# Kernel optimization log

Measured on AMD Instinct MI355X. Metric: run time of the kernel, lower is better.

Reference implementation:

```python
import jax, jax.numpy as jnp
import numpy as np
from jax import lax

N = 4096
T = 8192
DT = 0.1
C_M = 1.0
E_REST = 0.0
G_M_LEAK = 5.0
I_BIAS = 0.0


def setup_inputs() -> dict:
    key = jax.random.key(0)
    i_ext_vector = jax.random.normal(key, (N, T), dtype=jnp.float32)
    return {"i_ext_vector": i_ext_vector}


def reference(i_ext_vector) -> jnp.ndarray:
    # RK2 (modified Euler) integration of leaky non-spiking neuron dynamics.
    # dv/dt = (i_bias + i_ext - (v - e_rest) * g_m_leak) / c_m
    def dvdt(v, i_ext):
        return (I_BIAS + i_ext - (v - E_REST) * G_M_LEAK) / C_M

    def step(v, i_t):
        k1 = dvdt(v, i_t)
        k2 = dvdt(v + 0.5 * DT * k1, i_t)
        v_new = v + DT * k2
        return v_new, v_new

    v0 = jnp.full((N,), E_REST, dtype=i_ext_vector.dtype)
    # scan over time: i_ext_vector is (N, T) -> scan over leading axis of (T, N)
    _, v_hist = lax.scan(step, v0, i_ext_vector.T)  # v_hist: (T, N)
    return v_hist.T  # (N, T), matches v_m_Post
```

## Files before the change

kernel.cpp:

```cpp
#include <hip/hip_runtime.h>


typedef float fx4 __attribute__((ext_vector_type(4)));

constexpr int TT  = 8192;
constexpr int BLK = 256;
constexpr int SEG = 2048;
constexpr int NV  = 8;
constexpr int WPB = BLK / 64;

__global__ __launch_bounds__(BLK, 4)
void neuron_scan(const float* __restrict__ in, float* __restrict__ out,
                 int nseg) {
    const float A    = 0.625f;
    const float Bc   = 0.075f;
    const float A4   = 0.152587890625f;
    const float A8   = 2.32830643653869629e-2f;
    const float A16  = 5.42101086242752217e-4f;
    const float A32  = 2.93873587705571877e-7f;
    const float A64  = 8.63616855509444463e-14f;
    const float A128 = 7.45834073120020674e-27f;

    const int lane = threadIdx.x & 63;
    const int wid  = blockIdx.x * WPB + (threadIdx.x >> 6);
    const int nw   = gridDim.x * WPB;

    for (int s = wid; s < nseg; s += nw) {
        const int row = s >> 2;
        const int col = s & 3;
        const size_t base = (size_t)row * TT + (size_t)col * SEG;
        const fx4* src = (const fx4*)(in + base);

        fx4 x[NV];
        #pragma unroll
        for (int k = 0; k < NV; ++k) x[k] = src[NV * lane + k];

        const bool wu = (col > 0);
        fx4 wx = {0.0f, 0.0f, 0.0f, 0.0f};
        if (wu && lane < 16) wx = src[lane - 16];

        float c = 0.0f;
        #pragma unroll
        for (int k = 0; k < NV; ++k) {
            c = fmaf(A, c, Bc * x[k].x);
            c = fmaf(A, c, Bc * x[k].y);
            c = fmaf(A, c, Bc * x[k].z);
            c = fmaf(A, c, Bc * x[k].w);
        }

        float vwarm = 0.0f;
        if (wu) {
            float cw;
            cw = Bc * wx.x;
            cw = fmaf(A, cw, Bc * wx.y);
            cw = fmaf(A, cw, Bc * wx.z);
            cw = fmaf(A, cw, Bc * wx.w);
            float u;
            u = __shfl_up(cw, 1); if (lane >= 1) cw = fmaf(A4,  u, cw);
            u = __shfl_up(cw, 2); if (lane >= 2) cw = fmaf(A8,  u, cw);
            u = __shfl_up(cw, 4); if (lane >= 4) cw = fmaf(A16, u, cw);
            u = __shfl_up(cw, 8); if (lane >= 8) cw = fmaf(A32, u, cw);
            vwarm = __shfl(cw, 15);
        }
        if (lane == 0) c = fmaf(A32, vwarm, c);

        float u;
        u = __shfl_up(c, 1); if (lane >= 1) c = fmaf(A32,  u, c);
        u = __shfl_up(c, 2); if (lane >= 2) c = fmaf(A64,  u, c);
        u = __shfl_up(c, 4); if (lane >= 4) c = fmaf(A128, u, c);

        float venter = __shfl_up(c, 1);
        if (lane == 0) venter = vwarm;

        float v = venter;
        #pragma unroll
        for (int k = 0; k < NV; ++k) {
            v = fmaf(A, v, Bc * x[k].x); x[k].x = v;
            v = fmaf(A, v, Bc * x[k].y); x[k].y = v;
            v = fmaf(A, v, Bc * x[k].z); x[k].z = v;
            v = fmaf(A, v, Bc * x[k].w); x[k].w = v;
        }

        fx4* dst = (fx4*)(out + base);
        #pragma unroll
        for (int k = 0; k < NV; ++k) dst[NV * lane + k] = x[k];
    }
}

extern "C" void kernel_launch(void* const* d_in, const int* in_sizes, int n_in,
                              void* d_out, int out_size, void* d_ws, size_t ws_size,
                              hipStream_t stream) {
    const float* in = (const float*)d_in[0];
    float* out = (float*)d_out;
    const int n_rows = in_sizes[0] / TT;
    const int nseg = n_rows * (TT / SEG);
    int blocks = 1024;
    if (blocks * WPB > nseg) blocks = (nseg + WPB - 1) / WPB;
    neuron_scan<<<dim3(blocks), dim3(BLK), 0, stream>>>(in, out, nseg);
}
```

Before: 240.3 us.

## Software-pipeline segment loads and halve segment size per wavefront

Each wavefront now prefetches the next segment's inputs into registers before computing and storing the current one, so global load latency overlaps with the scan. Segment size drops from 2048 to 1024 (16 floats per lane), the shuffle-scan decay constants are adjusted to match, and the number of segments doubles. The double-buffered registers raise register use, so occupancy is lowered to 3 blocks per SIMD in the launch bounds. Smaller segments also mean more warm-up halo reads per row.

```diff
diff --git a/kernel.cpp b/kernel.cpp
--- a/kernel.cpp
+++ b/kernel.cpp
@@ -5,11 +5,11 @@
 
 constexpr int TT  = 8192;
 constexpr int BLK = 256;
-constexpr int SEG = 2048;
-constexpr int NV  = 8;
+constexpr int SEG = 1024;
+constexpr int NV  = 4;
 constexpr int WPB = BLK / 64;
 
-__global__ __launch_bounds__(BLK, 4)
+__global__ __launch_bounds__(BLK, 3)
 void neuron_scan(const float* __restrict__ in, float* __restrict__ out,
                  int nseg) {
     const float A    = 0.625f;
@@ -25,49 +25,59 @@
     const int wid  = blockIdx.x * WPB + (threadIdx.x >> 6);
     const int nw   = gridDim.x * WPB;
 
+    if (wid >= nseg) return;
+
+    fx4 xa[NV];
+    fx4 wxa = {0.0f, 0.0f, 0.0f, 0.0f};
+    {
+        const fx4* src = (const fx4*)(in + (size_t)wid * SEG);
+        #pragma unroll
+        for (int k = 0; k < NV; ++k) xa[k] = src[NV * lane + k];
+        if ((wid & 7) != 0 && lane < 16) wxa = src[lane - 16];
+    }
+
     for (int s = wid; s < nseg; s += nw) {
-        const int row = s >> 2;
-        const int col = s & 3;
-        const size_t base = (size_t)row * TT + (size_t)col * SEG;
-        const fx4* src = (const fx4*)(in + base);
-
-        fx4 x[NV];
-        #pragma unroll
-        for (int k = 0; k < NV; ++k) x[k] = src[NV * lane + k];
-
-        const bool wu = (col > 0);
-        fx4 wx = {0.0f, 0.0f, 0.0f, 0.0f};
-        if (wu && lane < 16) wx = src[lane - 16];
+        const int sn = s + nw;
+        fx4 xb[NV] = {};
+        fx4 wxb = {0.0f, 0.0f, 0.0f, 0.0f};
+        if (sn < nseg) {
+            const fx4* srcn = (const fx4*)(in + (size_t)sn * SEG);
+            #pragma unroll
+            for (int k = 0; k < NV; ++k) xb[k] = srcn[NV * lane + k];
+            if ((sn & 7) != 0 && lane < 16) wxb = srcn[lane - 16];
+        }
+        __builtin_amdgcn_sched_barrier(0);
 
         float c = 0.0f;
         #pragma unroll
         for (int k = 0; k < NV; ++k) {
-            c = fmaf(A, c, Bc * x[k].x);
-            c = fmaf(A, c, Bc * x[k].y);
-            c = fmaf(A, c, Bc * x[k].z);
-            c = fmaf(A, c, Bc * x[k].w);
+            c = fmaf(A, c, Bc * xa[k].x);
+            c = fmaf(A, c, Bc * xa[k].y);
+            c = fmaf(A, c, Bc * xa[k].z);
+            c = fmaf(A, c, Bc * xa[k].w);
         }
 
         float vwarm = 0.0f;
-        if (wu) {
+        if ((s & 7) != 0) {
             float cw;
-            cw = Bc * wx.x;
-            cw = fmaf(A, cw, Bc * wx.y);
-            cw = fmaf(A, cw, Bc * wx.z);
-            cw = fmaf(A, cw, Bc * wx.w);
-            float u;
-            u = __shfl_up(cw, 1); if (lane >= 1) cw = fmaf(A4,  u, cw);
-            u = __shfl_up(cw, 2); if (lane >= 2) cw = fmaf(A8,  u, cw);
-            u = __shfl_up(cw, 4); if (lane >= 4) cw = fmaf(A16, u, cw);
-            u = __shfl_up(cw, 8); if (lane >= 8) cw = fmaf(A32, u, cw);
+            cw = Bc * wxa.x;
+            cw = fmaf(A, cw, Bc * wxa.y);
+            cw = fmaf(A, cw, Bc * wxa.z);
+            cw = fmaf(A, cw, Bc * wxa.w);
+            float uw;
+            uw = __shfl_up(cw, 1); if (lane >= 1) cw = fmaf(A4,  uw, cw);
+            uw = __shfl_up(cw, 2); if (lane >= 2) cw = fmaf(A8,  uw, cw);
+            uw = __shfl_up(cw, 4); if (lane >= 4) cw = fmaf(A16, uw, cw);
+            uw = __shfl_up(cw, 8); if (lane >= 8) cw = fmaf(A32, uw, cw);
             vwarm = __shfl(cw, 15);
         }
-        if (lane == 0) c = fmaf(A32, vwarm, c);
+        if (lane == 0) c = fmaf(A16, vwarm, c);
 
         float u;
-        u = __shfl_up(c, 1); if (lane >= 1) c = fmaf(A32,  u, c);
-        u = __shfl_up(c, 2); if (lane >= 2) c = fmaf(A64,  u, c);
-        u = __shfl_up(c, 4); if (lane >= 4) c = fmaf(A128, u, c);
+        u = __shfl_up(c, 1); if (lane >= 1) c = fmaf(A16,  u, c);
+        u = __shfl_up(c, 2); if (lane >= 2) c = fmaf(A32,  u, c);
+        u = __shfl_up(c, 4); if (lane >= 4) c = fmaf(A64,  u, c);
+        u = __shfl_up(c, 8); if (lane >= 8) c = fmaf(A128, u, c);
 
         float venter = __shfl_up(c, 1);
         if (lane == 0) venter = vwarm;
@@ -75,15 +85,19 @@
         float v = venter;
         #pragma unroll
         for (int k = 0; k < NV; ++k) {
-            v = fmaf(A, v, Bc * x[k].x); x[k].x = v;
-            v = fmaf(A, v, Bc * x[k].y); x[k].y = v;
-            v = fmaf(A, v, Bc * x[k].z); x[k].z = v;
-            v = fmaf(A, v, Bc * x[k].w); x[k].w = v;
+            v = fmaf(A, v, Bc * xa[k].x); xa[k].x = v;
+            v = fmaf(A, v, Bc * xa[k].y); xa[k].y = v;
+            v = fmaf(A, v, Bc * xa[k].z); xa[k].z = v;
+            v = fmaf(A, v, Bc * xa[k].w); xa[k].w = v;
         }
 
-        fx4* dst = (fx4*)(out + base);
+        fx4* dst = (fx4*)(out + (size_t)s * SEG);
         #pragma unroll
-        for (int k = 0; k < NV; ++k) dst[NV * lane + k] = x[k];
+        for (int k = 0; k < NV; ++k) dst[NV * lane + k] = xa[k];
+
+        #pragma unroll
+        for (int k = 0; k < NV; ++k) xa[k] = xb[k];
+        wxa = wxb;
     }
 }
 
```

Result: no change. 237.8 us (-1.0%).
